# Performance work log

Measured on AMD Instinct MI355X. Metric: run time of the kernel, lower is better.

The kernel has to match this reference:

```python
import jax, jax.numpy as jnp
import numpy as np
import math
from jax import lax

B, C, H, DK, L, K, NCONV, P = 24, 128, 8, 16, 512, 7, 4, 0.1


def setup_inputs() -> dict:
    key = jax.random.key(0)
    ks = jax.random.split(key, 10)
    return {
        "x": jax.random.normal(ks[0], (B, C, L), jnp.float32),
        "dw_w": jax.random.normal(ks[1], (NCONV, C, 1, K), jnp.float32) * 0.1,
        "dw_b": jax.random.normal(ks[2], (NCONV, C), jnp.float32) * 0.1,
        "pw_w": jax.random.normal(ks[3], (NCONV, C, C, 1), jnp.float32) * 0.05,
        "pw_b": jax.random.normal(ks[4], (NCONV, C), jnp.float32) * 0.1,
        "Wq": jax.random.normal(ks[5], (H, B, DK, C), jnp.float32),
        "Wk": jax.random.normal(ks[6], (H, B, DK, C), jnp.float32),
        "Wv": jax.random.normal(ks[7], (H, B, DK, C), jnp.float32),
        "Wo": jax.random.normal(ks[8], (B, C, C), jnp.float32),
        "W": jax.random.normal(ks[9], (B, C, C), jnp.float32),
    }


def _norm(t, eps=1e-6):
    # torch: (x - mean) / (std + eps), std unbiased (ddof=1), over last (length) axis
    mean = t.mean(-1, keepdims=True)
    std = jnp.sqrt(((t - mean) ** 2).sum(-1, keepdims=True) / (t.shape[-1] - 1))
    return (t - mean) / (std + eps)


def _dropout(t, i):
    # deterministic dropout (training=True, p=0.1) with fixed per-call key
    keep = jax.random.bernoulli(jax.random.fold_in(jax.random.key(7), i), 1.0 - P, t.shape)
    return jnp.where(keep, t / (1.0 - P), jnp.zeros((), t.dtype))


def reference(x, dw_w, dw_b, pw_w, pw_b, Wq, Wk, Wv, Wo, W):
    # positional encoding: sin(sin(pos*freq + phase)) + x (note the double sin, faithful to source)
    i = np.arange(C)
    base = 10000.0 ** (-(i - (i % 2)) / C)
    freq = jnp.asarray(np.where(i % 2 == 0, base, -base), jnp.float32)
    phase = jnp.asarray(np.where(i % 2 == 0, 0.0, np.pi / 2), jnp.float32)
    pos = jnp.arange(L, dtype=jnp.float32)
    pe = jnp.sin(jnp.sin(pos[None, :] * freq[:, None] + phase[:, None]))  # (C, L)
    out = pe[None] + x
    res = out
    dn = ('NCH', 'OIH', 'NCH')
    for ci in range(NCONV):
        o = _norm(out)
        o = lax.conv_general_dilated(o, dw_w[ci], (1,), [(K // 2, K // 2)],
                                     feature_group_count=C, dimension_numbers=dn) + dw_b[ci][None, :, None]
        o = lax.conv_general_dilated(o, pw_w[ci], (1,), [(0, 0)],
                                     dimension_numbers=dn) + pw_b[ci][None, :, None]
        o = jax.nn.relu(o)
        out = _dropout(res + o, ci)
        res = out
    # self-attention (per-batch-element weight matrices, softmax over QUERY axis = torch dim=1)
    xn = _norm(out)
    q = jnp.einsum('hbkc,bcl->hbkl', Wq, xn)
    k = jnp.einsum('hbkc,bcl->hbkl', Wk, xn)
    v = jnp.einsum('hbkc,bcl->hbkl', Wv, xn)
    s = jnp.einsum('hbki,hbkj->hbij', q, k) / math.sqrt(DK)  # (H,B,L,L)
    p = jax.nn.softmax(s, axis=2)
    head = jnp.einsum('hbvi,hbij->hbvj', v, p)  # (H,B,DK,L)
    head = head.transpose(1, 0, 2, 3).reshape(B, H * DK, L)
    att = jnp.einsum('boc,bcl->bol', Wo, head)
    out = _dropout(res + att, NCONV)
    res = out
    # final per-batch projection + relu + residual
    o = jax.nn.relu(jnp.einsum('boc,bcl->bol', W, _norm(out)))
    out = _dropout(res + o, NCONV + 1)
    return out
```

## Files before the change

kernel.cpp:

```cpp
#include <hip/hip_runtime.h>
#include <stdint.h>
#include <math.h>

#define NB 24
#define NC 128
#define NH 8
#define NDK 16
#define NL 512
#define NTOT (24*128*512)

typedef float f32x4 __attribute__((ext_vector_type(4)));
typedef short s16x4 __attribute__((ext_vector_type(4)));

__device__ inline f32x4 mfma_bf16_16x16x16(s16x4 a, s16x4 b, f32x4 c) {
#if defined(__HIP_DEVICE_COMPILE__)
#if __has_builtin(__builtin_amdgcn_mfma_f32_16x16x16bf16_1k)
  return __builtin_amdgcn_mfma_f32_16x16x16bf16_1k(a, b, c, 0, 0, 0);
#else
  return __builtin_amdgcn_mfma_f32_16x16x16_bf16(a, b, c, 0, 0, 0);
#endif
#else
  (void)a; (void)b;
  return c;
#endif
}

__device__ inline unsigned short f2bf(float x) {
  uint32_t u = __float_as_uint(x);
  return (unsigned short)((u + 0x7FFFu + ((u >> 16) & 1u)) >> 16);
}
__device__ inline float bf2f(unsigned short s) {
  return __uint_as_float(((uint32_t)s) << 16);
}

__host__ __device__ inline void tf2x32(uint32_t k0, uint32_t k1, uint32_t& x0, uint32_t& x1) {
  uint32_t ks2 = k0 ^ k1 ^ 0x1BD11BDAu;
  x0 += k0; x1 += k1;
#define TF_R(r) { x0 += x1; x1 = (x1 << r) | (x1 >> (32 - r)); x1 ^= x0; }
  TF_R(13) TF_R(15) TF_R(26) TF_R(6)
  x0 += k1;  x1 += ks2 + 1u;
  TF_R(17) TF_R(29) TF_R(16) TF_R(24)
  x0 += ks2; x1 += k0 + 2u;
  TF_R(13) TF_R(15) TF_R(26) TF_R(6)
  x0 += k0;  x1 += k1 + 3u;
  TF_R(17) TF_R(29) TF_R(16) TF_R(24)
  x0 += k1;  x1 += ks2 + 4u;
  TF_R(13) TF_R(15) TF_R(26) TF_R(6)
  x0 += ks2; x1 += k0 + 5u;
#undef TF_R
}

__device__ inline float drop_scale(uint32_t k0, uint32_t k1, uint32_t idx) {
  uint32_t x0 = 0u, x1 = idx;
  tf2x32(k0, k1, x0, x1);
  uint32_t bits = x0 ^ x1;
  float u = __uint_as_float((bits >> 9) | 0x3f800000u) - 1.0f;
  return (u < 0.9f) ? (1.0f / 0.9f) : 0.0f;
}

__global__ __launch_bounds__(256) void pos_add_kernel(const float* __restrict__ x,
                                                      float* __restrict__ out) {
  int idx = blockIdx.x * 256 + threadIdx.x;
  int l = idx & (NL - 1);
  int c = (idx >> 9) & (NC - 1);
  int ce = c & ~1;
  double base = exp(-(double)ce * 9.210340371976184 / 128.0);
  float freq = (c & 1) ? -(float)base : (float)base;
  float phase = (c & 1) ? (float)(M_PI / 2.0) : 0.0f;
  float pe = sinf(sinf((float)l * freq + phase));
  out[idx] = x[idx] + pe;
}

template<bool DO_CONV>
__global__ __launch_bounds__(64) void norm_dw_kernel(const float* __restrict__ in,
                                                     float* __restrict__ outp,
                                                     const float* __restrict__ dww,
                                                     const float* __restrict__ dwb) {
  int row = blockIdx.x;
  int c = row & (NC - 1);
  int t = threadIdx.x;
  const float* rp = in + (size_t)row * NL;
  float4 v0 = ((const float4*)rp)[t * 2];
  float4 v1 = ((const float4*)rp)[t * 2 + 1];
  float xr[8] = {v0.x, v0.y, v0.z, v0.w, v1.x, v1.y, v1.z, v1.w};
  float s = 0.f;
#pragma unroll
  for (int j = 0; j < 8; ++j) s += xr[j];
#pragma unroll
  for (int off = 32; off >= 1; off >>= 1) s += __shfl_xor(s, off);
  float mean = s * (1.0f / 512.0f);
  float sq = 0.f;
#pragma unroll
  for (int j = 0; j < 8; ++j) { xr[j] -= mean; sq += xr[j] * xr[j]; }
#pragma unroll
  for (int off = 32; off >= 1; off >>= 1) sq += __shfl_xor(sq, off);
  float inv = 1.0f / (sqrtf(sq * (1.0f / 511.0f)) + 1e-6f);

  if (!DO_CONV) {
    float4 o0 = make_float4(xr[0]*inv, xr[1]*inv, xr[2]*inv, xr[3]*inv);
    float4 o1 = make_float4(xr[4]*inv, xr[5]*inv, xr[6]*inv, xr[7]*inv);
    float4* op = (float4*)(outp + (size_t)row * NL);
    op[t * 2] = o0; op[t * 2 + 1] = o1;
  } else {
    __shared__ float rb[NL + 6];
    if (t < 3) { rb[t] = 0.f; rb[NL + 3 + t] = 0.f; }
#pragma unroll
    for (int j = 0; j < 8; ++j) rb[3 + t * 8 + j] = xr[j] * inv;
    __syncthreads();
    float w[7];
#pragma unroll
    for (int u = 0; u < 7; ++u) w[u] = dww[c * 7 + u];
    float bias = dwb[c];
    float* op = outp + (size_t)row * NL + t * 8;
#pragma unroll
    for (int j = 0; j < 8; ++j) {
      int l = t * 8 + j;
      float o = bias;
#pragma unroll
      for (int u = 0; u < 7; ++u) o += rb[l + u] * w[u];
      op[j] = o;
    }
  }
}

template<int EPI, bool A_PER_B>
__global__ __launch_bounds__(256) void gemm_mfma_kernel(const float* __restrict__ A,
                                                        const float* __restrict__ X,
                                                        float* __restrict__ Y,
                                                        const float* __restrict__ bias,
                                                        const float* __restrict__ resid,
                                                        uint32_t k0, uint32_t k1) {
  __shared__ unsigned short Ah[64][68], Al[64][68];
  __shared__ unsigned short Xh[64][68], Xl[64][68];
  int b  = blockIdx.z;
  int m0 = blockIdx.y * 64;
  int l0 = blockIdx.x * 64;
  int t  = threadIdx.x;
  const int lane = t & 63, w = t >> 6;
  const int g = lane >> 4, j16 = lane & 15;
  const float* Ab = A + (A_PER_B ? (size_t)b * NC * NC : 0);
  const float* Xb = X + (size_t)b * NC * NL;

  f32x4 acc[4] = {{0.f,0.f,0.f,0.f},{0.f,0.f,0.f,0.f},{0.f,0.f,0.f,0.f},{0.f,0.f,0.f,0.f}};

  for (int kc = 0; kc < 2; ++kc) {
#pragma unroll
    for (int i = 0; i < 4; ++i) {
      int id = t + i * 256;
      int r = id >> 4, c4 = (id & 15) << 2;
      float4 v = *(const float4*)&Ab[(size_t)(m0 + r) * NC + kc * 64 + c4];
      unsigned short h0 = f2bf(v.x), h1 = f2bf(v.y), h2 = f2bf(v.z), h3 = f2bf(v.w);
      Ah[r][c4] = h0; Ah[r][c4+1] = h1; Ah[r][c4+2] = h2; Ah[r][c4+3] = h3;
      Al[r][c4]   = f2bf(v.x - bf2f(h0));
      Al[r][c4+1] = f2bf(v.y - bf2f(h1));
      Al[r][c4+2] = f2bf(v.z - bf2f(h2));
      Al[r][c4+3] = f2bf(v.w - bf2f(h3));
    }
    {
      int n = t & 63, kbase = (t >> 6) * 16;
#pragma unroll
      for (int kk = 0; kk < 16; ++kk) {
        float v = Xb[(size_t)(kc * 64 + kbase + kk) * NL + l0 + n];
        unsigned short hi = f2bf(v);
        Xh[n][kbase + kk] = hi;
        Xl[n][kbase + kk] = f2bf(v - bf2f(hi));
      }
    }
    __syncthreads();
#pragma unroll
    for (int ks = 0; ks < 4; ++ks) {
      int ko = ks * 16 + 4 * g;
      s16x4 a_h = *(const s16x4*)&Ah[w * 16 + j16][ko];
      s16x4 a_l = *(const s16x4*)&Al[w * 16 + j16][ko];
#pragma unroll
      for (int nt = 0; nt < 4; ++nt) {
        s16x4 x_h = *(const s16x4*)&Xh[nt * 16 + j16][ko];
        s16x4 x_l = *(const s16x4*)&Xl[nt * 16 + j16][ko];
        acc[nt] = mfma_bf16_16x16x16(a_h, x_h, acc[nt]);
        acc[nt] = mfma_bf16_16x16x16(a_l, x_h, acc[nt]);
        acc[nt] = mfma_bf16_16x16x16(a_h, x_l, acc[nt]);
      }
    }
    __syncthreads();
  }

#pragma unroll
  for (int nt = 0; nt < 4; ++nt) {
    int n = l0 + nt * 16 + j16;
#pragma unroll
    for (int r = 0; r < 4; ++r) {
      int m = m0 + w * 16 + 4 * g + r;
      float val = acc[nt][r] + ((EPI == 0) ? bias[m] : 0.0f);
      if (EPI == 0 || EPI == 2) val = fmaxf(val, 0.0f);
      size_t idx = ((size_t)b * NC + m) * NL + n;
      float v2 = resid[idx] + val;
      float ds = drop_scale(k0, k1, (uint32_t)idx);
      Y[idx] = (ds == 0.0f) ? 0.0f : (v2 / 0.9f);
    }
  }
}

__global__ __launch_bounds__(256) void qkv_mfma_kernel(const float* __restrict__ Wq,
                                                       const float* __restrict__ Wk,
                                                       const float* __restrict__ Wv,
                                                       const float* __restrict__ X,
                                                       unsigned short* __restrict__ qhw,
                                                       unsigned short* __restrict__ qlw,
                                                       unsigned short* __restrict__ khw,
                                                       unsigned short* __restrict__ klw,
                                                       unsigned short* __restrict__ vbw) {
  __shared__ unsigned short Ah[64][68], Al[64][68];
  __shared__ unsigned short Xh[64][68], Xl[64][68];
  int b  = blockIdx.z;
  int m0 = blockIdx.y * 64;
  int l0 = blockIdx.x * 64;
  int t  = threadIdx.x;
  const int lane = t & 63, w = t >> 6;
  const int g = lane >> 4, j16 = lane & 15;
  const int sel = m0 >> 7;
  const float* Wp = (sel == 0) ? Wq : ((sel == 1) ? Wk : Wv);
  const float* Xb = X + (size_t)b * NC * NL;

  f32x4 acc[4] = {{0.f,0.f,0.f,0.f},{0.f,0.f,0.f,0.f},{0.f,0.f,0.f,0.f},{0.f,0.f,0.f,0.f}};

  for (int kc = 0; kc < 2; ++kc) {
#pragma unroll
    for (int i = 0; i < 4; ++i) {
      int id = t + i * 256;
      int r = id >> 4, c4 = (id & 15) << 2;
      int gr = m0 + r;
      int w_ = gr & 127, h = w_ >> 4, kk = w_ & 15;
      const float* rowp = Wp + (((size_t)h * NB + b) * NDK + kk) * NC + kc * 64;
      float4 v = *(const float4*)&rowp[c4];
      unsigned short h0 = f2bf(v.x), h1 = f2bf(v.y), h2 = f2bf(v.z), h3 = f2bf(v.w);
      Ah[r][c4] = h0; Ah[r][c4+1] = h1; Ah[r][c4+2] = h2; Ah[r][c4+3] = h3;
      Al[r][c4]   = f2bf(v.x - bf2f(h0));
      Al[r][c4+1] = f2bf(v.y - bf2f(h1));
      Al[r][c4+2] = f2bf(v.z - bf2f(h2));
      Al[r][c4+3] = f2bf(v.w - bf2f(h3));
    }
    {
      int n = t & 63, kbase = (t >> 6) * 16;
#pragma unroll
      for (int kk = 0; kk < 16; ++kk) {
        float v = Xb[(size_t)(kc * 64 + kbase + kk) * NL + l0 + n];
        unsigned short hi = f2bf(v);
        Xh[n][kbase + kk] = hi;
        Xl[n][kbase + kk] = f2bf(v - bf2f(hi));
      }
    }
    __syncthreads();
#pragma unroll
    for (int ks = 0; ks < 4; ++ks) {
      int ko = ks * 16 + 4 * g;
      s16x4 a_h = *(const s16x4*)&Ah[w * 16 + j16][ko];
      s16x4 a_l = *(const s16x4*)&Al[w * 16 + j16][ko];
#pragma unroll
      for (int nt = 0; nt < 4; ++nt) {
        s16x4 x_h = *(const s16x4*)&Xh[nt * 16 + j16][ko];
        s16x4 x_l = *(const s16x4*)&Xl[nt * 16 + j16][ko];
        acc[nt] = mfma_bf16_16x16x16(a_h, x_h, acc[nt]);
        acc[nt] = mfma_bf16_16x16x16(a_l, x_h, acc[nt]);
        acc[nt] = mfma_bf16_16x16x16(a_h, x_l, acc[nt]);
      }
    }
    __syncthreads();
  }

#pragma unroll
  for (int nt = 0; nt < 4; ++nt) {
    int n = l0 + nt * 16 + j16;
#pragma unroll
    for (int r = 0; r < 4; ++r) {
      int grow = m0 + w * 16 + 4 * g + r;
      int w_ = grow & 127, h = w_ >> 4, kk = w_ & 15;
      size_t idx = (((size_t)h * NB + b) * NDK + kk) * NL + n;
      float v = acc[nt][r];
      if (sel == 0) {
        float s = v * 0.25f;
        unsigned short hi = f2bf(s);
        qhw[idx] = hi; qlw[idx] = f2bf(s - bf2f(hi));
      } else if (sel == 1) {
        unsigned short hi = f2bf(v);
        khw[idx] = hi; klw[idx] = f2bf(v - bf2f(hi));
      } else {
        vbw[idx] = f2bf(v);
      }
    }
  }
}

__global__ __launch_bounds__(256) void attn_kernel(const unsigned short* __restrict__ qh,
                                                   const unsigned short* __restrict__ ql,
                                                   const unsigned short* __restrict__ kh,
                                                   const unsigned short* __restrict__ kl,
                                                   const unsigned short* __restrict__ vb,
                                                   float* __restrict__ headbuf) {
  __shared__ unsigned short KtH[128][16], KtL[128][16];
  __shared__ unsigned short QtH[2][16][16], QtL[2][16][16], Vt[2][16][16];
  const int t = threadIdx.x;
  const int lane = t & 63, w = t >> 6;
  const int g = lane >> 4, j16 = lane & 15;
  const int hb = blockIdx.y, jq = blockIdx.x;
  const int j0 = jq * 128;
  const int h = hb / NB, b = hb % NB;
  const size_t kb = (size_t)hb * NDK * NL;

  {
    int j = t & 127, k8 = (t >> 7) * 8;
#pragma unroll
    for (int kk = 0; kk < 8; ++kk) {
      KtH[j][k8 + kk] = kh[kb + (size_t)(k8 + kk) * NL + j0 + j];
      KtL[j][k8 + kk] = kl[kb + (size_t)(k8 + kk) * NL + j0 + j];
    }
  }
  {
    int k_ = t >> 4, i_ = t & 15;
    size_t src = kb + (size_t)k_ * NL + i_;
    QtH[0][i_][k_] = qh[src];
    QtL[0][i_][k_] = ql[src];
    Vt [0][k_][i_] = vb[src];
  }
  __syncthreads();

  s16x4 KhiF[2], KloF[2];
#pragma unroll
  for (int q = 0; q < 2; ++q) {
    int jj = (w * 2 + q) * 16 + j16;
    KhiF[q] = *(const s16x4*)&KtH[jj][4 * g];
    KloF[q] = *(const s16x4*)&KtL[jj][4 * g];
  }

  float Mq[2] = {-INFINITY, -INFINITY};
  float lq[2] = {0.f, 0.f};
  f32x4 hC[2] = {{0.f, 0.f, 0.f, 0.f}, {0.f, 0.f, 0.f, 0.f}};

  int buf = 0;
  for (int it = 0; it < 32; ++it) {
    if (it < 31) {
      int k_ = t >> 4, i_ = t & 15, nb = buf ^ 1;
      size_t src = kb + (size_t)k_ * NL + (it + 1) * 16 + i_;
      QtH[nb][i_][k_] = qh[src];
      QtL[nb][i_][k_] = ql[src];
      Vt [nb][k_][i_] = vb[src];
    }
    s16x4 Qhi = *(const s16x4*)&QtH[buf][j16][4 * g];
    s16x4 Qlo = *(const s16x4*)&QtL[buf][j16][4 * g];
    s16x4 Vf  = *(const s16x4*)&Vt [buf][j16][4 * g];
#pragma unroll
    for (int q = 0; q < 2; ++q) {
      f32x4 S = {0.f, 0.f, 0.f, 0.f};
      S = mfma_bf16_16x16x16(Qhi, KhiF[q], S);
      S = mfma_bf16_16x16x16(Qlo, KhiF[q], S);
      S = mfma_bf16_16x16x16(Qhi, KloF[q], S);
      float tm = fmaxf(fmaxf(S[0], S[1]), fmaxf(S[2], S[3]));
      tm = fmaxf(tm, __shfl_xor(tm, 16));
      tm = fmaxf(tm, __shfl_xor(tm, 32));
      float Mn = fmaxf(Mq[q], tm);
      float corr = __expf(Mq[q] - Mn);
      Mq[q] = Mn;
      float p0 = __expf(S[0] - Mn), p1 = __expf(S[1] - Mn);
      float p2 = __expf(S[2] - Mn), p3 = __expf(S[3] - Mn);
      lq[q] = lq[q] * corr + ((p0 + p1) + (p2 + p3));
      hC[q] = hC[q] * corr;
      union { uint32_t u[2]; s16x4 s; } bp;
      bp.u[0] = (uint32_t)f2bf(p0) | ((uint32_t)f2bf(p1) << 16);
      bp.u[1] = (uint32_t)f2bf(p2) | ((uint32_t)f2bf(p3) << 16);
      hC[q] = mfma_bf16_16x16x16(Vf, bp.s, hC[q]);
    }
    __syncthreads();
    buf ^= 1;
  }

#pragma unroll
  for (int q = 0; q < 2; ++q) {
    float l2 = lq[q] + __shfl_xor(lq[q], 16);
    float L  = l2 + __shfl_xor(l2, 32);
    float invL = 1.0f / L;
    int jglob = j0 + (w * 2 + q) * 16 + j16;
    float* hp = headbuf + ((size_t)b * NC + h * NDK + 4 * g) * NL + jglob;
    hp[0 * NL] = hC[q][0] * invL;
    hp[1 * NL] = hC[q][1] * invL;
    hp[2 * NL] = hC[q][2] * invL;
    hp[3 * NL] = hC[q][3] * invL;
  }
}

extern "C" void kernel_launch(void* const* d_in, const int* in_sizes, int n_in,
                              void* d_out, int out_size, void* d_ws, size_t ws_size,
                              hipStream_t stream) {
  (void)in_sizes; (void)n_in; (void)out_size; (void)ws_size;
  const float* x    = (const float*)d_in[0];
  const float* dw_w = (const float*)d_in[1];
  const float* dw_b = (const float*)d_in[2];
  const float* pw_w = (const float*)d_in[3];
  const float* pw_b = (const float*)d_in[4];
  const float* Wq   = (const float*)d_in[5];
  const float* Wk   = (const float*)d_in[6];
  const float* Wv   = (const float*)d_in[7];
  const float* Wo   = (const float*)d_in[8];
  const float* W    = (const float*)d_in[9];
  float* out = (float*)d_out;

  const size_t N = NTOT;
  float* cur  = (float*)d_ws;
  float* bufA = cur + N;
  float* bufB = bufA + N;
  unsigned short* qh = (unsigned short*)(bufB + N);
  unsigned short* ql = qh + N;
  unsigned short* kh = ql + N;
  unsigned short* kl = kh + N;
  unsigned short* vb = kl + N;

  uint32_t fk0[6], fk1[6];
  for (int i = 0; i < 6; ++i) {
    uint32_t a = 0u, bb = (uint32_t)i;
    tf2x32(0u, 7u, a, bb);
    fk0[i] = a; fk1[i] = bb;
  }

  pos_add_kernel<<<NTOT / 256, 256, 0, stream>>>(x, cur);

  for (int ci = 0; ci < 4; ++ci) {
    norm_dw_kernel<true><<<NB * NC, 64, 0, stream>>>(cur, bufB, dw_w + ci * NC * 7, dw_b + ci * NC);
    gemm_mfma_kernel<0, false><<<dim3(8, 2, NB), 256, 0, stream>>>(
        pw_w + (size_t)ci * NC * NC, bufB, cur, pw_b + ci * NC, cur, fk0[ci], fk1[ci]);
  }

  norm_dw_kernel<false><<<NB * NC, 64, 0, stream>>>(cur, bufA, nullptr, nullptr);
  qkv_mfma_kernel<<<dim3(8, 6, NB), 256, 0, stream>>>(Wq, Wk, Wv, bufA, qh, ql, kh, kl, vb);
  attn_kernel<<<dim3(4, NH * NB), 256, 0, stream>>>(qh, ql, kh, kl, vb, bufB);
  gemm_mfma_kernel<1, true><<<dim3(8, 2, NB), 256, 0, stream>>>(
      Wo, bufB, cur, nullptr, cur, fk0[4], fk1[4]);

  norm_dw_kernel<false><<<NB * NC, 64, 0, stream>>>(cur, bufA, nullptr, nullptr);
  gemm_mfma_kernel<2, true><<<dim3(8, 2, NB), 256, 0, stream>>>(
      W, bufA, out, nullptr, cur, fk0[5], fk1[5]);
}
```

Measured before the change: 208.3 us.

## Pre-split weights and activations to bf16 hi/lo in producers, fuse pos-enc into norm

Adds a prep kernel that splits all weight matrices into bf16 hi/lo pairs once per call. The norm/conv and attention kernels now emit bf16 hi/lo activations directly, so the GEMMs load ready-made bf16 tiles instead of converting fp32 in their inner loops. Positional encoding is folded into the first norm kernel, which removes a separate pass. The attention kernel loads all Q and V for the head into LDS up front, dropping the per-iteration double buffer and its barriers, at the cost of more LDS and lower occupancy.

```diff
diff --git a/kernel.cpp b/kernel.cpp
--- a/kernel.cpp
+++ b/kernel.cpp
@@ -58,22 +58,46 @@
   return (u < 0.9f) ? (1.0f / 0.9f) : 0.0f;
 }
 
-__global__ __launch_bounds__(256) void pos_add_kernel(const float* __restrict__ x,
-                                                      float* __restrict__ out) {
+#define S0 (4*128*128)
+#define SW (24*128*128)
+#define SQ (8*24*16*128)
+#define oPwH 0
+#define oPwL (S0)
+#define oWoH (2*S0)
+#define oWoL (2*S0 + SW)
+#define oWH  (2*S0 + 2*SW)
+#define oWL  (2*S0 + 3*SW)
+#define oQH  (2*S0 + 4*SW)
+#define oQL  (2*S0 + 4*SW + SQ)
+#define oKH  (2*S0 + 4*SW + 2*SQ)
+#define oKL  (2*S0 + 4*SW + 3*SQ)
+#define oVH  (2*S0 + 4*SW + 4*SQ)
+#define oVL  (2*S0 + 4*SW + 5*SQ)
+#define PREP_TOT (S0 + 2*SW + 3*SQ)
+
+__global__ __launch_bounds__(256) void prep_split_kernel(
+    const float* __restrict__ pw_w, const float* __restrict__ Wo, const float* __restrict__ W,
+    const float* __restrict__ Wq, const float* __restrict__ Wk, const float* __restrict__ Wv,
+    unsigned short* __restrict__ ws) {
   int idx = blockIdx.x * 256 + threadIdx.x;
-  int l = idx & (NL - 1);
-  int c = (idx >> 9) & (NC - 1);
-  int ce = c & ~1;
-  double base = exp(-(double)ce * 9.210340371976184 / 128.0);
-  float freq = (c & 1) ? -(float)base : (float)base;
-  float phase = (c & 1) ? (float)(M_PI / 2.0) : 0.0f;
-  float pe = sinf(sinf((float)l * freq + phase));
-  out[idx] = x[idx] + pe;
-}
-
-template<bool DO_CONV>
+  const float* src; unsigned short *dh, *dl; int off;
+  if (idx < S0)                { src = pw_w; dh = ws + oPwH; dl = ws + oPwL; off = idx; }
+  else if (idx < S0 + SW)      { src = Wo;   dh = ws + oWoH; dl = ws + oWoL; off = idx - S0; }
+  else if (idx < S0 + 2*SW)    { src = W;    dh = ws + oWH;  dl = ws + oWL;  off = idx - S0 - SW; }
+  else if (idx < S0 + 2*SW + SQ)   { src = Wq; dh = ws + oQH; dl = ws + oQL; off = idx - S0 - 2*SW; }
+  else if (idx < S0 + 2*SW + 2*SQ) { src = Wk; dh = ws + oKH; dl = ws + oKL; off = idx - S0 - 2*SW - SQ; }
+  else                             { src = Wv; dh = ws + oVH; dl = ws + oVL; off = idx - S0 - 2*SW - 2*SQ; }
+  float v = src[off];
+  unsigned short hi = f2bf(v);
+  dh[off] = hi;
+  dl[off] = f2bf(v - bf2f(hi));
+}
+
+template<bool DO_CONV, bool ADD_PE>
 __global__ __launch_bounds__(64) void norm_dw_kernel(const float* __restrict__ in,
-                                                     float* __restrict__ outp,
+                                                     float* __restrict__ cur_out,
+                                                     unsigned short* __restrict__ oh,
+                                                     unsigned short* __restrict__ ol,
                                                      const float* __restrict__ dww,
                                                      const float* __restrict__ dwb) {
   int row = blockIdx.x;
@@ -83,6 +107,19 @@
   float4 v0 = ((const float4*)rp)[t * 2];
   float4 v1 = ((const float4*)rp)[t * 2 + 1];
   float xr[8] = {v0.x, v0.y, v0.z, v0.w, v1.x, v1.y, v1.z, v1.w};
+  if (ADD_PE) {
+    int ce = c & ~1;
+    double base = exp(-(double)ce * 9.210340371976184 / 128.0);
+    float freq = (c & 1) ? -(float)base : (float)base;
+    float phase = (c & 1) ? (float)(M_PI / 2.0) : 0.0f;
+#pragma unroll
+    for (int j = 0; j < 8; ++j)
+      xr[j] += sinf(sinf((float)(t * 8 + j) * freq + phase));
+    float4 o0 = make_float4(xr[0], xr[1], xr[2], xr[3]);
+    float4 o1 = make_float4(xr[4], xr[5], xr[6], xr[7]);
+    float4* cp = (float4*)(cur_out + (size_t)row * NL);
+    cp[t * 2] = o0; cp[t * 2 + 1] = o1;
+  }
   float s = 0.f;
 #pragma unroll
   for (int j = 0; j < 8; ++j) s += xr[j];
@@ -96,11 +133,15 @@
   for (int off = 32; off >= 1; off >>= 1) sq += __shfl_xor(sq, off);
   float inv = 1.0f / (sqrtf(sq * (1.0f / 511.0f)) + 1e-6f);
 
+  size_t obase = (size_t)row * NL + t * 8;
   if (!DO_CONV) {
-    float4 o0 = make_float4(xr[0]*inv, xr[1]*inv, xr[2]*inv, xr[3]*inv);
-    float4 o1 = make_float4(xr[4]*inv, xr[5]*inv, xr[6]*inv, xr[7]*inv);
-    float4* op = (float4*)(outp + (size_t)row * NL);
-    op[t * 2] = o0; op[t * 2 + 1] = o1;
+#pragma unroll
+    for (int j = 0; j < 8; ++j) {
+      float o = xr[j] * inv;
+      unsigned short hi = f2bf(o);
+      oh[obase + j] = hi;
+      ol[obase + j] = f2bf(o - bf2f(hi));
+    }
   } else {
     __shared__ float rb[NL + 6];
     if (t < 3) { rb[t] = 0.f; rb[NL + 3 + t] = 0.f; }
@@ -111,25 +152,25 @@
 #pragma unroll
     for (int u = 0; u < 7; ++u) w[u] = dww[c * 7 + u];
     float bias = dwb[c];
-    float* op = outp + (size_t)row * NL + t * 8;
 #pragma unroll
     for (int j = 0; j < 8; ++j) {
       int l = t * 8 + j;
       float o = bias;
 #pragma unroll
       for (int u = 0; u < 7; ++u) o += rb[l + u] * w[u];
-      op[j] = o;
+      unsigned short hi = f2bf(o);
+      oh[obase + j] = hi;
+      ol[obase + j] = f2bf(o - bf2f(hi));
     }
   }
 }
 
 template<int EPI, bool A_PER_B>
-__global__ __launch_bounds__(256) void gemm_mfma_kernel(const float* __restrict__ A,
-                                                        const float* __restrict__ X,
-                                                        float* __restrict__ Y,
-                                                        const float* __restrict__ bias,
-                                                        const float* __restrict__ resid,
-                                                        uint32_t k0, uint32_t k1) {
+__global__ __launch_bounds__(256) void gemm_mfma_kernel(
+    const unsigned short* __restrict__ AhB, const unsigned short* __restrict__ AlB,
+    const unsigned short* __restrict__ XhB, const unsigned short* __restrict__ XlB,
+    float* __restrict__ Y, const float* __restrict__ bias, const float* __restrict__ resid,
+    uint32_t k0, uint32_t k1) {
   __shared__ unsigned short Ah[64][68], Al[64][68];
   __shared__ unsigned short Xh[64][68], Xl[64][68];
   int b  = blockIdx.z;
@@ -138,8 +179,9 @@
   int t  = threadIdx.x;
   const int lane = t & 63, w = t >> 6;
   const int g = lane >> 4, j16 = lane & 15;
-  const float* Ab = A + (A_PER_B ? (size_t)b * NC * NC : 0);
-  const float* Xb = X + (size_t)b * NC * NL;
+  const unsigned short* Abh = AhB + (A_PER_B ? (size_t)b * NC * NC : 0);
+  const unsigned short* Abl = AlB + (A_PER_B ? (size_t)b * NC * NC : 0);
+  const size_t xb = (size_t)b * NC * NL;
 
   f32x4 acc[4] = {{0.f,0.f,0.f,0.f},{0.f,0.f,0.f,0.f},{0.f,0.f,0.f,0.f},{0.f,0.f,0.f,0.f}};
 
@@ -147,23 +189,18 @@
 #pragma unroll
     for (int i = 0; i < 4; ++i) {
       int id = t + i * 256;
-      int r = id >> 4, c4 = (id & 15) << 2;
-      float4 v = *(const float4*)&Ab[(size_t)(m0 + r) * NC + kc * 64 + c4];
-      unsigned short h0 = f2bf(v.x), h1 = f2bf(v.y), h2 = f2bf(v.z), h3 = f2bf(v.w);
-      Ah[r][c4] = h0; Ah[r][c4+1] = h1; Ah[r][c4+2] = h2; Ah[r][c4+3] = h3;
-      Al[r][c4]   = f2bf(v.x - bf2f(h0));
-      Al[r][c4+1] = f2bf(v.y - bf2f(h1));
-      Al[r][c4+2] = f2bf(v.z - bf2f(h2));
-      Al[r][c4+3] = f2bf(v.w - bf2f(h3));
+      int r = id >> 4, u = (id & 15) << 2;
+      *(s16x4*)&Ah[r][u] = *(const s16x4*)&Abh[(size_t)(m0 + r) * NC + kc * 64 + u];
+      *(s16x4*)&Al[r][u] = *(const s16x4*)&Abl[(size_t)(m0 + r) * NC + kc * 64 + u];
     }
     {
-      int n = t & 63, kbase = (t >> 6) * 16;
+      int n = t & 63, kq = (t >> 6) * 16;
 #pragma unroll
       for (int kk = 0; kk < 16; ++kk) {
-        float v = Xb[(size_t)(kc * 64 + kbase + kk) * NL + l0 + n];
-        unsigned short hi = f2bf(v);
-        Xh[n][kbase + kk] = hi;
-        Xl[n][kbase + kk] = f2bf(v - bf2f(hi));
+        int k = kq + kk;
+        size_t src = xb + (size_t)(kc * 64 + k) * NL + l0 + n;
+        Xh[n][k] = XhB[src];
+        Xl[n][k] = XlB[src];
       }
     }
     __syncthreads();
@@ -200,15 +237,12 @@
   }
 }
 
-__global__ __launch_bounds__(256) void qkv_mfma_kernel(const float* __restrict__ Wq,
-                                                       const float* __restrict__ Wk,
-                                                       const float* __restrict__ Wv,
-                                                       const float* __restrict__ X,
-                                                       unsigned short* __restrict__ qhw,
-                                                       unsigned short* __restrict__ qlw,
-                                                       unsigned short* __restrict__ khw,
-                                                       unsigned short* __restrict__ klw,
-                                                       unsigned short* __restrict__ vbw) {
+__global__ __launch_bounds__(256) void qkv_mfma_kernel(
+    const unsigned short* __restrict__ wsp,
+    const unsigned short* __restrict__ XhB, const unsigned short* __restrict__ XlB,
+    unsigned short* __restrict__ qhw, unsigned short* __restrict__ qlw,
+    unsigned short* __restrict__ khw, unsigned short* __restrict__ klw,
+    unsigned short* __restrict__ vbw) {
   __shared__ unsigned short Ah[64][68], Al[64][68];
   __shared__ unsigned short Xh[64][68], Xl[64][68];
   int b  = blockIdx.z;
@@ -218,8 +252,9 @@
   const int lane = t & 63, w = t >> 6;
   const int g = lane >> 4, j16 = lane & 15;
   const int sel = m0 >> 7;
-  const float* Wp = (sel == 0) ? Wq : ((sel == 1) ? Wk : Wv);
-  const float* Xb = X + (size_t)b * NC * NL;
+  const unsigned short* WpH = wsp + ((sel == 0) ? oQH : (sel == 1) ? oKH : oVH);
+  const unsigned short* WpL = wsp + ((sel == 0) ? oQL : (sel == 1) ? oKL : oVL);
+  const size_t xb = (size_t)b * NC * NL;
 
   f32x4 acc[4] = {{0.f,0.f,0.f,0.f},{0.f,0.f,0.f,0.f},{0.f,0.f,0.f,0.f},{0.f,0.f,0.f,0.f}};
 
@@ -227,26 +262,21 @@
 #pragma unroll
     for (int i = 0; i < 4; ++i) {
       int id = t + i * 256;
-      int r = id >> 4, c4 = (id & 15) << 2;
+      int r = id >> 4, u = (id & 15) << 2;
       int gr = m0 + r;
       int w_ = gr & 127, h = w_ >> 4, kk = w_ & 15;
-      const float* rowp = Wp + (((size_t)h * NB + b) * NDK + kk) * NC + kc * 64;
-      float4 v = *(const float4*)&rowp[c4];
-      unsigned short h0 = f2bf(v.x), h1 = f2bf(v.y), h2 = f2bf(v.z), h3 = f2bf(v.w);
-      Ah[r][c4] = h0; Ah[r][c4+1] = h1; Ah[r][c4+2] = h2; Ah[r][c4+3] = h3;
-      Al[r][c4]   = f2bf(v.x - bf2f(h0));
-      Al[r][c4+1] = f2bf(v.y - bf2f(h1));
-      Al[r][c4+2] = f2bf(v.z - bf2f(h2));
-      Al[r][c4+3] = f2bf(v.w - bf2f(h3));
+      size_t rowoff = (((size_t)h * NB + b) * NDK + kk) * NC + kc * 64 + u;
+      *(s16x4*)&Ah[r][u] = *(const s16x4*)&WpH[rowoff];
+      *(s16x4*)&Al[r][u] = *(const s16x4*)&WpL[rowoff];
     }
     {
-      int n = t & 63, kbase = (t >> 6) * 16;
+      int n = t & 63, kq = (t >> 6) * 16;
 #pragma unroll
       for (int kk = 0; kk < 16; ++kk) {
-        float v = Xb[(size_t)(kc * 64 + kbase + kk) * NL + l0 + n];
-        unsigned short hi = f2bf(v);
-        Xh[n][kbase + kk] = hi;
-        Xl[n][kbase + kk] = f2bf(v - bf2f(hi));
+        int k = kq + kk;
+        size_t src = xb + (size_t)(kc * 64 + k) * NL + l0 + n;
+        Xh[n][k] = XhB[src];
+        Xl[n][k] = XlB[src];
       }
     }
     __syncthreads();
@@ -277,9 +307,9 @@
       size_t idx = (((size_t)h * NB + b) * NDK + kk) * NL + n;
       float v = acc[nt][r];
       if (sel == 0) {
-        float s = v * 0.25f;
-        unsigned short hi = f2bf(s);
-        qhw[idx] = hi; qlw[idx] = f2bf(s - bf2f(hi));
+        float sv = v * 0.25f;
+        unsigned short hi = f2bf(sv);
+        qhw[idx] = hi; qlw[idx] = f2bf(sv - bf2f(hi));
       } else if (sel == 1) {
         unsigned short hi = f2bf(v);
         khw[idx] = hi; klw[idx] = f2bf(v - bf2f(hi));
@@ -295,9 +325,11 @@
                                                    const unsigned short* __restrict__ kh,
                                                    const unsigned short* __restrict__ kl,
                                                    const unsigned short* __restrict__ vb,
-                                                   float* __restrict__ headbuf) {
+                                                   unsigned short* __restrict__ oh,
+                                                   unsigned short* __restrict__ ol) {
+  __shared__ unsigned short QtH[512][16], QtL[512][16];
   __shared__ unsigned short KtH[128][16], KtL[128][16];
-  __shared__ unsigned short QtH[2][16][16], QtL[2][16][16], Vt[2][16][16];
+  __shared__ unsigned short Vt[16][520];
   const int t = threadIdx.x;
   const int lane = t & 63, w = t >> 6;
   const int g = lane >> 4, j16 = lane & 15;
@@ -306,20 +338,22 @@
   const int h = hb / NB, b = hb % NB;
   const size_t kb = (size_t)hb * NDK * NL;
 
-  {
-    int j = t & 127, k8 = (t >> 7) * 8;
-#pragma unroll
-    for (int kk = 0; kk < 8; ++kk) {
-      KtH[j][k8 + kk] = kh[kb + (size_t)(k8 + kk) * NL + j0 + j];
-      KtL[j][k8 + kk] = kl[kb + (size_t)(k8 + kk) * NL + j0 + j];
-    }
-  }
-  {
-    int k_ = t >> 4, i_ = t & 15;
-    size_t src = kb + (size_t)k_ * NL + i_;
-    QtH[0][i_][k_] = qh[src];
-    QtL[0][i_][k_] = ql[src];
-    Vt [0][k_][i_] = vb[src];
+  for (int n = 0; n < 32; ++n) {
+    int e = n * 256 + t;
+    int k = e >> 9, i = e & 511;
+    QtH[i][k] = qh[kb + (size_t)k * NL + i];
+    QtL[i][k] = ql[kb + (size_t)k * NL + i];
+  }
+  for (int n = 0; n < 16; ++n) {
+    int e = n * 256 + t;
+    int v = e >> 8, i2 = e & 255;
+    *(uint32_t*)&Vt[v][i2 * 2] = *(const uint32_t*)&vb[kb + (size_t)v * NL + i2 * 2];
+  }
+  for (int n = 0; n < 8; ++n) {
+    int e = n * 256 + t;
+    int k = e >> 7, j = e & 127;
+    KtH[j][k] = kh[kb + (size_t)k * NL + j0 + j];
+    KtL[j][k] = kl[kb + (size_t)k * NL + j0 + j];
   }
   __syncthreads();
 
@@ -335,18 +369,10 @@
   float lq[2] = {0.f, 0.f};
   f32x4 hC[2] = {{0.f, 0.f, 0.f, 0.f}, {0.f, 0.f, 0.f, 0.f}};
 
-  int buf = 0;
   for (int it = 0; it < 32; ++it) {
-    if (it < 31) {
-      int k_ = t >> 4, i_ = t & 15, nb = buf ^ 1;
-      size_t src = kb + (size_t)k_ * NL + (it + 1) * 16 + i_;
-      QtH[nb][i_][k_] = qh[src];
-      QtL[nb][i_][k_] = ql[src];
-      Vt [nb][k_][i_] = vb[src];
-    }
-    s16x4 Qhi = *(const s16x4*)&QtH[buf][j16][4 * g];
-    s16x4 Qlo = *(const s16x4*)&QtL[buf][j16][4 * g];
-    s16x4 Vf  = *(const s16x4*)&Vt [buf][j16][4 * g];
+    s16x4 Qhi = *(const s16x4*)&QtH[it * 16 + j16][4 * g];
+    s16x4 Qlo = *(const s16x4*)&QtL[it * 16 + j16][4 * g];
+    s16x4 Vf  = *(const s16x4*)&Vt[j16][it * 16 + 4 * g];
 #pragma unroll
     for (int q = 0; q < 2; ++q) {
       f32x4 S = {0.f, 0.f, 0.f, 0.f};
@@ -368,8 +394,6 @@
       bp.u[1] = (uint32_t)f2bf(p2) | ((uint32_t)f2bf(p3) << 16);
       hC[q] = mfma_bf16_16x16x16(Vf, bp.s, hC[q]);
     }
-    __syncthreads();
-    buf ^= 1;
   }
 
 #pragma unroll
@@ -378,11 +402,14 @@
     float L  = l2 + __shfl_xor(l2, 32);
     float invL = 1.0f / L;
     int jglob = j0 + (w * 2 + q) * 16 + j16;
-    float* hp = headbuf + ((size_t)b * NC + h * NDK + 4 * g) * NL + jglob;
-    hp[0 * NL] = hC[q][0] * invL;
-    hp[1 * NL] = hC[q][1] * invL;
-    hp[2 * NL] = hC[q][2] * invL;
-    hp[3 * NL] = hC[q][3] * invL;
+#pragma unroll
+    for (int r = 0; r < 4; ++r) {
+      float val = hC[q][r] * invL;
+      size_t idx = ((size_t)b * NC + h * NDK + 4 * g + r) * NL + jglob;
+      unsigned short hi = f2bf(val);
+      oh[idx] = hi;
+      ol[idx] = f2bf(val - bf2f(hi));
+    }
   }
 }
 
@@ -403,14 +430,15 @@
   float* out = (float*)d_out;
 
   const size_t N = NTOT;
-  float* cur  = (float*)d_ws;
-  float* bufA = cur + N;
-  float* bufB = bufA + N;
-  unsigned short* qh = (unsigned short*)(bufB + N);
-  unsigned short* ql = qh + N;
-  unsigned short* kh = ql + N;
-  unsigned short* kl = kh + N;
-  unsigned short* vb = kl + N;
+  float* cur = (float*)d_ws;
+  unsigned short* XhB = (unsigned short*)(cur + N);
+  unsigned short* XlB = XhB + N;
+  unsigned short* qh  = XlB + N;
+  unsigned short* ql  = qh + N;
+  unsigned short* kh  = ql + N;
+  unsigned short* kl  = kh + N;
+  unsigned short* vb  = kl + N;
+  unsigned short* wsp = vb + N;
 
   uint32_t fk0[6], fk1[6];
   for (int i = 0; i < 6; ++i) {
@@ -419,21 +447,26 @@
     fk0[i] = a; fk1[i] = bb;
   }
 
-  pos_add_kernel<<<NTOT / 256, 256, 0, stream>>>(x, cur);
-
-  for (int ci = 0; ci < 4; ++ci) {
-    norm_dw_kernel<true><<<NB * NC, 64, 0, stream>>>(cur, bufB, dw_w + ci * NC * 7, dw_b + ci * NC);
+  prep_split_kernel<<<PREP_TOT / 256, 256, 0, stream>>>(pw_w, Wo, W, Wq, Wk, Wv, wsp);
+
+  norm_dw_kernel<true, true><<<NB * NC, 64, 0, stream>>>(x, cur, XhB, XlB, dw_w, dw_b);
+  gemm_mfma_kernel<0, false><<<dim3(8, 2, NB), 256, 0, stream>>>(
+      wsp + oPwH, wsp + oPwL, XhB, XlB, cur, pw_b, cur, fk0[0], fk1[0]);
+  for (int ci = 1; ci < 4; ++ci) {
+    norm_dw_kernel<true, false><<<NB * NC, 64, 0, stream>>>(cur, nullptr, XhB, XlB,
+                                                            dw_w + ci * NC * 7, dw_b + ci * NC);
     gemm_mfma_kernel<0, false><<<dim3(8, 2, NB), 256, 0, stream>>>(
-        pw_w + (size_t)ci * NC * NC, bufB, cur, pw_b + ci * NC, cur, fk0[ci], fk1[ci]);
-  }
-
-  norm_dw_kernel<false><<<NB * NC, 64, 0, stream>>>(cur, bufA, nullptr, nullptr);
-  qkv_mfma_kernel<<<dim3(8, 6, NB), 256, 0, stream>>>(Wq, Wk, Wv, bufA, qh, ql, kh, kl, vb);
-  attn_kernel<<<dim3(4, NH * NB), 256, 0, stream>>>(qh, ql, kh, kl, vb, bufB);
+        wsp + oPwH + (size_t)ci * NC * NC, wsp + oPwL + (size_t)ci * NC * NC,
+        XhB, XlB, cur, pw_b + ci * NC, cur, fk0[ci], fk1[ci]);
+  }
+
+  norm_dw_kernel<false, false><<<NB * NC, 64, 0, stream>>>(cur, nullptr, XhB, XlB, nullptr, nullptr);
+  qkv_mfma_kernel<<<dim3(8, 6, NB), 256, 0, stream>>>(wsp, XhB, XlB, qh, ql, kh, kl, vb);
+  attn_kernel<<<dim3(4, NH * NB), 256, 0, stream>>>(qh, ql, kh, kl, vb, XhB, XlB);
   gemm_mfma_kernel<1, true><<<dim3(8, 2, NB), 256, 0, stream>>>(
-      Wo, bufB, cur, nullptr, cur, fk0[4], fk1[4]);
-
-  norm_dw_kernel<false><<<NB * NC, 64, 0, stream>>>(cur, bufA, nullptr, nullptr);
+      wsp + oWoH, wsp + oWoL, XhB, XlB, cur, nullptr, cur, fk0[4], fk1[4]);
+
+  norm_dw_kernel<false, false><<<NB * NC, 64, 0, stream>>>(cur, nullptr, XhB, XlB, nullptr, nullptr);
   gemm_mfma_kernel<2, true><<<dim3(8, 2, NB), 256, 0, stream>>>(
-      W, bufA, out, nullptr, cur, fk0[5], fk1[5]);
-}
+      wsp + oWH, wsp + oWL, XhB, XlB, out, nullptr, cur, fk0[5], fk1[5]);
+}
```

New measurement: 186.6 us. -10.4%, faster.
